# Optimization experiments

Hardware: AMD Instinct MI355X
Metric: run time of the kernel (lower is better)

## Reference

```python
import jax, jax.numpy as jnp
import numpy as np

SCALE, R_MAX, ALPHA = 16, 8, 2.0
HL, WL, C_FEAT = 16, 16, 384
HH, WH = HL * SCALE, WL * SCALE


def bilinear_resize(img, out_h, out_w):
    """PyTorch F.interpolate(mode='bilinear', align_corners=False, antialias=False).
    img: [..., H, W] -> [..., out_h, out_w]."""
    H, W = img.shape[-2], img.shape[-1]
    ys = jnp.maximum((jnp.arange(out_h, dtype=jnp.float32) + 0.5) * (H / out_h) - 0.5, 0.0)
    xs = jnp.maximum((jnp.arange(out_w, dtype=jnp.float32) + 0.5) * (W / out_w) - 0.5, 0.0)
    y0 = jnp.floor(ys).astype(jnp.int32)
    x0 = jnp.floor(xs).astype(jnp.int32)
    y1 = jnp.minimum(y0 + 1, H - 1)
    x1 = jnp.minimum(x0 + 1, W - 1)
    wy = (ys - y0)[:, None]
    wx = (xs - x0)[None, :]
    g = lambda yi, xi: img[..., yi[:, None], xi[None, :]]
    return ((1 - wy) * (1 - wx) * g(y0, x0) + (1 - wy) * wx * g(y0, x1)
            + wy * (1 - wx) * g(y1, x0) + wy * wx * g(y1, x1))


def jbu_forward(feat_lr, guide_hr, sx_raw, sy_raw, th_raw, sr_raw):
    C, Hl, Wl = feat_lr.shape[1], feat_lr.shape[2], feat_lr.shape[3]
    Hh, Wh = guide_hr.shape[2], guide_hr.shape[3]
    scale, R_max, alpha = SCALE, R_MAX, ALPHA
    NEG = -1e30  # finite stand-in for -inf (keeps grads NaN-free)

    # parameter transforms from the module
    sx = jnp.exp(sx_raw[0, 0])
    sy = jnp.exp(sy_raw[0, 0])
    th = jnp.pi * jnp.tanh(th_raw[0, 0])
    sr = jnp.exp(sr_raw[0, 0])

    Y, X = jnp.meshgrid(jnp.arange(Hh, dtype=jnp.float32),
                        jnp.arange(Wh, dtype=jnp.float32), indexing='ij')
    u = (Y + 0.5) / scale - 0.5
    v = (X + 0.5) / scale - 0.5
    uc = jnp.clip(jnp.round(u), 0, Hl - 1).astype(jnp.int32)
    vc = jnp.clip(jnp.round(v), 0, Wl - 1).astype(jnp.int32)

    sigma_eff_hr = bilinear_resize(jnp.maximum(sx, sy), Hh, Wh)
    R_map = jnp.clip(jnp.ceil(alpha * sigma_eff_hr), 1.0, float(R_max))  # [Hh,Wh]

    offs = jnp.arange(-R_max, R_max + 1, dtype=jnp.int32)
    dYg, dXg = jnp.meshgrid(offs, offs, indexing='ij')
    dY = dYg.reshape(-1)[:, None, None]  # [N,1,1]
    dX = dXg.reshape(-1)[:, None, None]

    Ui = jnp.clip(uc[None] + dY, 0, Hl - 1)  # [N,Hh,Wh]
    Vi = jnp.clip(vc[None] + dX, 0, Wl - 1)
    idx = Ui * Wl + Vi                       # flat LR index per (neighbor, HR pixel)
    gat = lambda mp: mp.reshape(-1)[idx]

    sxg = jnp.maximum(gat(sx), 1e-6)
    syg = jnp.maximum(gat(sy), 1e-6)
    thg = gat(th)
    srg = jnp.maximum(gat(sr), 1e-6)

    dx = X[None] - ((Vi.astype(jnp.float32) + 0.5) * scale - 0.5)
    dyv = Y[None] - ((Ui.astype(jnp.float32) + 0.5) * scale - 0.5)
    ct, st = jnp.cos(thg), jnp.sin(thg)
    a = dx * ct + dyv * st
    b = -dx * st + dyv * ct

    guide_lr = bilinear_resize(guide_hr[0], Hl, Wl)  # [3,Hl,Wl]
    g_diff2 = sum((guide_hr[0, c][None] - gat(guide_lr[c])) ** 2 for c in range(3))

    log_w = (-a * a / (2 * sxg ** 2 + 1e-8)
             - b * b / (2 * syg ** 2 + 1e-8)
             - g_diff2 / (2.0 * srg ** 2 + 1e-8))  # [N,Hh,Wh]

    mask = (dY * dY + dX * dX).astype(jnp.float32) <= R_map[None] ** 2
    log_w = jnp.where(mask, log_w, NEG)

    # numerically stable softmax over neighbors (== online-softmax result)
    m = log_w.max(axis=0)
    s = jnp.exp(log_w - m[None])  # masked entries underflow to 0
    den = s.sum(axis=0)           # [Hh,Wh]

    # num[c,h,w] = sum_n s[n,h,w] * feat[idx[n,h,w], c]
    # scatter neighbor weights by LR pixel, then one GEMM with the LR features
    N = idx.shape[0]
    idx2 = idx.reshape(N, Hh * Wh)
    cols = jnp.arange(Hh * Wh, dtype=jnp.int32)[None, :]
    acc = jnp.zeros((Hl * Wl, Hh * Wh), jnp.float32).at[idx2, cols].add(s.reshape(N, -1))
    feat_flat = feat_lr[0].reshape(C, Hl * Wl)  # [C, P]
    num = jnp.einsum('cp,pq->cq', feat_flat, acc).reshape(C, Hh, Wh)

    return (num / jnp.maximum(den, 1e-8)[None])[None]  # [1,C,Hh,Wh]


def setup_inputs() -> dict:
    key = jax.random.key(0)
    k1, k2, k3, k4, k5, k6 = jax.random.split(key, 6)
    feat_lr = jax.random.normal(k1, (1, C_FEAT, HL, WL), jnp.float32)
    guide_hr = jax.random.uniform(k2, (1, 3, HH, WH), dtype=jnp.float32)
    log_sigma = float(np.log(16.0))
    log_sigma_r = float(np.log(0.12))
    sx_raw = log_sigma + 0.1 * jax.random.normal(k3, (1, 1, HL, WL), jnp.float32)
    sy_raw = log_sigma + 0.1 * jax.random.normal(k4, (1, 1, HL, WL), jnp.float32)
    th_raw = 0.1 * jax.random.normal(k5, (1, 1, HL, WL), jnp.float32)
    sr_raw = log_sigma_r + 0.1 * jax.random.normal(k6, (1, 1, HL, WL), jnp.float32)
    return {"feat_lr": feat_lr, "guide_hr": guide_hr, "sx_raw": sx_raw,
            "sy_raw": sy_raw, "th_raw": th_raw, "sr_raw": sr_raw}


def reference(feat_lr, guide_hr, sx_raw, sy_raw, th_raw, sr_raw):
    return jbu_forward(feat_lr, guide_hr, sx_raw, sy_raw, th_raw, sr_raw)
```

## Files before the change

kernel.cpp:

```cpp
#include <hip/hip_runtime.h>
#include <math.h>

#define NEG_BIG  (-1e30f)
#define NEG_H16  (-60000.0f)

typedef _Float16 half8  __attribute__((ext_vector_type(8)));
typedef _Float16 half2v __attribute__((ext_vector_type(2)));
typedef float    floatx4 __attribute__((ext_vector_type(4)));

__global__ __launch_bounds__(256) void setup_all(
    const float* __restrict__ feat, const float* __restrict__ guide,
    const float* __restrict__ sx_raw, const float* __restrict__ sy_raw,
    const float* __restrict__ th_raw, const float* __restrict__ sr_raw,
    _Float16* __restrict__ feat16, float4* __restrict__ PA,
    float4* __restrict__ PB, float* __restrict__ PS,
    _Float16* __restrict__ LCtab)
{
    const int b = blockIdx.x, t = threadIdx.x;
    if (b < 48) {
        int i = (b*256 + t)*8;
        float4 f0 = *(const float4*)(feat + i);
        float4 f1 = *(const float4*)(feat + i + 4);
        half8 h;
        h[0]=(_Float16)f0.x; h[1]=(_Float16)f0.y; h[2]=(_Float16)f0.z; h[3]=(_Float16)f0.w;
        h[4]=(_Float16)f1.x; h[5]=(_Float16)f1.y; h[6]=(_Float16)f1.z; h[7]=(_Float16)f1.w;
        *(half8*)(feat16 + i) = h;
        return;
    }
    if (b == 48) {
        float sx = expf(sx_raw[t]);
        float sy = expf(sy_raw[t]);
        float th = 3.14159265358979323846f * tanhf(th_raw[t]);
        float sr = expf(sr_raw[t]);
        float sxg = fmaxf(sx, 1e-6f), syg = fmaxf(sy, 1e-6f), srg = fmaxf(sr, 1e-6f);
        float iA = 1.f / (2.f*sxg*sxg + 1e-8f);
        float iB = 1.f / (2.f*syg*syg + 1e-8f);
        float iC = 1.f / (2.f*srg*srg + 1e-8f);
        float ct = cosf(th), st = sinf(th);
        float A2 = iA*ct*ct + iB*st*st;
        float B2 = 2.f*ct*st*(iA - iB);
        float C2 = iA*st*st + iB*ct*ct;
        PA[t] = make_float4(-A2, -B2, -C2, -iC);
        int i = t >> 4, j = t & 15;
        int y0 = 16*i + 7, x0 = 16*j + 7;
        float g[3];
#pragma unroll
        for (int c = 0; c < 3; ++c) {
            const float* gp = guide + c*65536;
            g[c] = 0.25f*(gp[y0*256 + x0]     + gp[y0*256 + x0 + 1] +
                          gp[(y0+1)*256 + x0] + gp[(y0+1)*256 + x0 + 1]);
        }
        PB[t] = make_float4(2.f*iC*g[0], 2.f*iC*g[1], 2.f*iC*g[2],
                            -iC*(g[0]*g[0] + g[1]*g[1] + g[2]*g[2]));
        PS[t] = fmaxf(sx, sy);
        return;
    }
    const int tb  = b - 49;
    const int uc  = tb >> 2;
    const int vc0 = (tb & 3) << 2;
    const int Pu  = t >> 4;
    const int colb = t & 15;
    int ylo = (Pu == 0)  ? -8 : (Pu - uc);
    int yhi = (Pu == 15) ?  8 : (Pu - uc);
    ylo = max(ylo, -8); yhi = min(yhi, 8);
    _Float16* dst = LCtab + (size_t)tb * 8192;
#pragma unroll
    for (int h = 0; h < 2; ++h) {
        const int col32 = colb + h*16;
        const int Rt = (col32 >> 2) + 1;
        const int vc = vc0 + (col32 & 3);
        const int R2 = Rt * Rt;
        int cnt[16];
#pragma unroll
        for (int Pv = 1; Pv < 15; ++Pv) {
            int d = Pv - vc;
            int lim = R2 - d*d;
            int c = 0;
            if (lim >= 0 && ylo <= yhi) {
                int s = (int)sqrtf((float)lim);
                c = max(0, min(yhi, s) - max(ylo, -s) + 1);
            }
            cnt[Pv] = c;
        }
        cnt[0] = 0;
        if (-vc >= -8) {
            for (int dY = ylo; dY <= yhi; ++dY) {
                int lim = R2 - dY*dY;
                if (lim >= 0) {
                    int r = (int)sqrtf((float)lim);
                    cnt[0] += max(0, min(-vc, r) + r + 1);
                }
            }
        }
        cnt[15] = 0;
        if (15 - vc <= 8) {
            for (int dY = ylo; dY <= yhi; ++dY) {
                int lim = R2 - dY*dY;
                if (lim >= 0) {
                    int r = (int)sqrtf((float)lim);
                    cnt[15] += max(0, r - max(15 - vc, -r) + 1);
                }
            }
        }
#pragma unroll
        for (int Pv = 0; Pv < 16; ++Pv)
            dst[(Pu*16 + Pv)*32 + col32] = (_Float16)
                ((cnt[Pv] > 0) ? __logf((float)cnt[Pv]) : NEG_H16);
    }
}

__global__ __launch_bounds__(1024, 8) void jbu_main(
    const float* __restrict__ guide, const _Float16* __restrict__ feat16,
    const float4* __restrict__ PA, const float4* __restrict__ PB,
    const float* __restrict__ PS, const _Float16* __restrict__ LCtab,
    float* __restrict__ out)
{
    __shared__ __align__(16) _Float16 Wb[64][256];
    __shared__ float redM[16][64];
    __shared__ float redD[16][64];

    const int t  = threadIdx.x;
    const int q  = t & 63;
    const int wv = t >> 6;
    const int grpu = __builtin_amdgcn_readfirstlane(wv);

    const int n   = blockIdx.x;
    const int xcd = n & 7;
    const int s   = n >> 3;
    const int Y   = xcd*32 + (s >> 2);
    const int X0  = (s & 3) << 6;
    const int X   = X0 + q;
    const float Yf = (float)Y, Xf = (float)X;
    const int uc   = Y >> 4;

    float u = (Yf + 0.5f)*0.0625f - 0.5f;
    float v = (Xf + 0.5f)*0.0625f - 0.5f;
    float ysc = fmaxf(u, 0.f), xsc = fmaxf(v, 0.f);
    int y0 = (int)ysc, x0 = (int)xsc;
    int y1 = min(y0 + 1, 15), x1 = min(x0 + 1, 15);
    float wy = ysc - (float)y0, wx = xsc - (float)x0;
    float s00 = PS[y0*16 + x0], s01 = PS[y0*16 + x1];
    float s10 = PS[y1*16 + x0], s11 = PS[y1*16 + x1];
    float sig = (1.f - wy)*((1.f - wx)*s00 + wx*s01)
              +        wy *((1.f - wx)*s10 + wx*s11);
    float Rf = fminf(fmaxf(ceilf(2.f*sig), 1.f), 8.f);
    const int colq = ((int)Rf - 1)*4 + (q >> 4);

    const float g0 = guide[          (Y << 8) + X];
    const float g1 = guide[ 65536 + ((Y << 8) + X)];
    const float g2 = guide[131072 + ((Y << 8) + X)];
    const float g2s = g0*g0 + g1*g1 + g2*g2;

    const _Float16* Lb = LCtab + (size_t)(uc*4 + (X0 >> 6))*8192 + colq;

    const int pbase = grpu << 4;
    const float dy  = Yf - (16.f*(float)grpu + 7.5f);
    const float dy2 = dy*dy;
    float lw[16];
    float mloc = NEG_BIG;
#pragma unroll
    for (int col = 0; col < 16; ++col) {
        int p = pbase + col;
        float dx = Xf - (16.f*(float)col + 7.5f);
        float4 A = PA[p];
        float4 B = PB[p];
        float w = fmaf(B.x, g0, B.w);
        w = fmaf(B.y, g1, w);
        w = fmaf(B.z, g2, w);
        w = fmaf(A.w, g2s, w);
        w = fmaf(A.x, dx*dx, w);
        w = fmaf(A.y, dx*dy, w);
        w = fmaf(A.z, dy2, w);
        w += (float)Lb[p*32];
        lw[col] = w;
        mloc = fmaxf(mloc, w);
    }
    redM[wv][q] = mloc;
    __syncthreads();
    float m = redM[0][q];
#pragma unroll
    for (int k = 1; k < 16; ++k) m = fmaxf(m, redM[k][q]);

    float dloc = 0.f;
#pragma unroll
    for (int col = 0; col < 16; col += 2) {
        int p0 = pbase + col;
        float e0 = __expf(lw[col]     - m);
        float e1 = __expf(lw[col + 1] - m);
        half2v hh; hh[0] = (_Float16)e0; hh[1] = (_Float16)e1;
        int chunk = ((p0 >> 3) ^ q) & 31;
        *(half2v*)&Wb[q][chunk*8 + (p0 & 7)] = hh;
        dloc += (float)hh[0] + (float)hh[1];
    }
    redD[wv][q] = dloc;
    __syncthreads();

    const int lane = t & 63;
    const int mrow = lane & 15;
    const int quad = lane >> 4;
    const int cg   = grpu >> 1;
    const int ph   = grpu & 1;
    const int c0   = cg * 48;
    const int pixbase = ph * 32;

    float idv[2];
#pragma unroll
    for (int nt = 0; nt < 2; ++nt) {
        int pix = pixbase + nt*16 + mrow;
        float den = 0.f;
#pragma unroll
        for (int k = 0; k < 16; ++k) den += redD[k][pix];
        idv[nt] = 1.f / fmaxf(den, 1e-8f);
    }

    floatx4 acc[3][2] = {};
    const _Float16* fbase = feat16 + (c0 + mrow)*256 + quad*8;

#pragma unroll
    for (int ks = 0; ks < 8; ++ks) {
        half8 a[3];
#pragma unroll
        for (int mt = 0; mt < 3; ++mt)
            a[mt] = *(const half8*)(fbase + mt*16*256 + ks*32);
        half8 b[2];
#pragma unroll
        for (int nt = 0; nt < 2; ++nt) {
            int pix = pixbase + nt*16 + mrow;
            int chunk = ((ks*4 + quad) ^ pix) & 31;
            b[nt] = *(const half8*)(&Wb[pix][chunk*8]);
        }
#pragma unroll
        for (int mt = 0; mt < 3; ++mt)
#pragma unroll
            for (int nt = 0; nt < 2; ++nt)
                acc[mt][nt] = __builtin_amdgcn_mfma_f32_16x16x32_f16(
                    a[mt], b[nt], acc[mt][nt], 0, 0, 0);
    }

    __syncthreads();

    float* Sf = (float*)Wb + (grpu << 9);
    const int sch = lane >> 3;
    const int spg = lane & 7;
    const int outcol = (Y << 8) + X0 + pixbase;
#pragma unroll
    for (int mt = 0; mt < 3; ++mt) {
#pragma unroll
        for (int nt = 0; nt < 2; ++nt)
#pragma unroll
            for (int r = 0; r < 4; ++r)
                Sf[(quad*4 + r)*32 + nt*16 + mrow] = acc[mt][nt][r] * idv[nt];
#pragma unroll
        for (int j = 0; j < 2; ++j) {
            float4 vv = *(const float4*)&Sf[(j*8 + sch)*32 + spg*4];
            *(float4*)(out + (size_t)(c0 + mt*16 + j*8 + sch)*65536
                           + outcol + spg*4) = vv;
        }
    }
}

extern "C" void kernel_launch(void* const* d_in, const int* in_sizes, int n_in,
                              void* d_out, int out_size, void* d_ws, size_t ws_size,
                              hipStream_t stream)
{
    const float* feat   = (const float*)d_in[0];
    const float* guide  = (const float*)d_in[1];
    const float* sx_raw = (const float*)d_in[2];
    const float* sy_raw = (const float*)d_in[3];
    const float* th_raw = (const float*)d_in[4];
    const float* sr_raw = (const float*)d_in[5];
    float* out = (float*)d_out;

    char* ws = (char*)d_ws;
    _Float16* feat16 = (_Float16*)ws;
    float4*   PA     = (float4*)(ws + 196608);
    float4*   PB     = (float4*)(ws + 200704);
    float*    PS     = (float*)(ws + 204800);
    _Float16* LCtab  = (_Float16*)(ws + 205824);

    setup_all<<<113, 256, 0, stream>>>(feat, guide, sx_raw, sy_raw, th_raw,
                                       sr_raw, feat16, PA, PB, PS, LCtab);
    jbu_main<<<1024, 1024, 0, stream>>>(guide, feat16, PA, PB, PS, LCtab, out);
}
```

Before: 164.4 us.

## Split fused JBU kernel into weight-generation and GEMM kernels via global buffer

Splits the single fused kernel into two. The first computes the per-pixel softmax weights and inverse denominators and writes them to a 32 MB fp16 global buffer. The second performs the feature-by-weight MFMA GEMM per HR row with wider output tiles and row-contiguous stores. This aims to let each phase have its own occupancy and tiling and to write output more coalesced, at the cost of a large extra global write and read of the weights plus an additional launch.

Result: slower. 185.3 us (+12.7%).

```diff
diff --git a/kernel.cpp b/kernel.cpp
--- a/kernel.cpp
+++ b/kernel.cpp
@@ -109,11 +109,11 @@
     }
 }
 
-__global__ __launch_bounds__(1024, 8) void jbu_main(
-    const float* __restrict__ guide, const _Float16* __restrict__ feat16,
-    const float4* __restrict__ PA, const float4* __restrict__ PB,
-    const float* __restrict__ PS, const _Float16* __restrict__ LCtab,
-    float* __restrict__ out)
+__global__ __launch_bounds__(1024) void jbu_wden(
+    const float* __restrict__ guide, const float4* __restrict__ PA,
+    const float4* __restrict__ PB, const float* __restrict__ PS,
+    const _Float16* __restrict__ LCtab,
+    _Float16* __restrict__ Wg, float* __restrict__ invden)
 {
     __shared__ __align__(16) _Float16 Wb[64][256];
     __shared__ float redM[16][64];
@@ -125,10 +125,8 @@
     const int grpu = __builtin_amdgcn_readfirstlane(wv);
 
     const int n   = blockIdx.x;
-    const int xcd = n & 7;
-    const int s   = n >> 3;
-    const int Y   = xcd*32 + (s >> 2);
-    const int X0  = (s & 3) << 6;
+    const int Y   = n >> 2;
+    const int X0  = (n & 3) << 6;
     const int X   = X0 + q;
     const float Yf = (float)Y, Xf = (float)X;
     const int uc   = Y >> 4;
@@ -195,66 +193,99 @@
     redD[wv][q] = dloc;
     __syncthreads();
 
+    if (t < 64) {
+        float den = 0.f;
+#pragma unroll
+        for (int k = 0; k < 16; ++k) den += redD[k][t];
+        invden[(Y << 8) + X0 + t] = 1.f / fmaxf(den, 1e-8f);
+    }
+
+    {
+        const float4* src = (const float4*)((const char*)Wb + t*32);
+        float4* dst = (float4*)((char*)Wg
+                        + ((size_t)(Y << 8) + (size_t)X0)*512 + (size_t)t*32);
+        dst[0] = src[0];
+        dst[1] = src[1];
+    }
+}
+
+__global__ __launch_bounds__(1024) void jbu_gemm(
+    const _Float16* __restrict__ feat16, const _Float16* __restrict__ Wg,
+    const float* __restrict__ invden, float* __restrict__ out)
+{
+    __shared__ float Sf[32*264];
+
+    const int t    = threadIdx.x;
     const int lane = t & 63;
+    const int wv   = t >> 6;
     const int mrow = lane & 15;
     const int quad = lane >> 4;
-    const int cg   = grpu >> 1;
-    const int ph   = grpu & 1;
-    const int c0   = cg * 48;
-    const int pixbase = ph * 32;
-
-    float idv[2];
-#pragma unroll
-    for (int nt = 0; nt < 2; ++nt) {
-        int pix = pixbase + nt*16 + mrow;
-        float den = 0.f;
-#pragma unroll
-        for (int k = 0; k < 16; ++k) den += redD[k][pix];
-        idv[nt] = 1.f / fmaxf(den, 1e-8f);
-    }
-
-    floatx4 acc[3][2] = {};
-    const _Float16* fbase = feat16 + (c0 + mrow)*256 + quad*8;
-
-#pragma unroll
-    for (int ks = 0; ks < 8; ++ks) {
-        half8 a[3];
-#pragma unroll
-        for (int mt = 0; mt < 3; ++mt)
-            a[mt] = *(const half8*)(fbase + mt*16*256 + ks*32);
-        half8 b[2];
-#pragma unroll
-        for (int nt = 0; nt < 2; ++nt) {
-            int pix = pixbase + nt*16 + mrow;
-            int chunk = ((ks*4 + quad) ^ pix) & 31;
-            b[nt] = *(const half8*)(&Wb[pix][chunk*8]);
-        }
-#pragma unroll
-        for (int mt = 0; mt < 3; ++mt)
-#pragma unroll
-            for (int nt = 0; nt < 2; ++nt)
-                acc[mt][nt] = __builtin_amdgcn_mfma_f32_16x16x32_f16(
-                    a[mt], b[nt], acc[mt][nt], 0, 0, 0);
-    }
-
-    __syncthreads();
-
-    float* Sf = (float*)Wb + (grpu << 9);
-    const int sch = lane >> 3;
-    const int spg = lane & 7;
-    const int outcol = (Y << 8) + X0 + pixbase;
-#pragma unroll
-    for (int mt = 0; mt < 3; ++mt) {
-#pragma unroll
-        for (int nt = 0; nt < 2; ++nt)
-#pragma unroll
-            for (int r = 0; r < 4; ++r)
-                Sf[(quad*4 + r)*32 + nt*16 + mrow] = acc[mt][nt][r] * idv[nt];
-#pragma unroll
-        for (int j = 0; j < 2; ++j) {
-            float4 vv = *(const float4*)&Sf[(j*8 + sch)*32 + spg*4];
-            *(float4*)(out + (size_t)(c0 + mt*16 + j*8 + sch)*65536
-                           + outcol + spg*4) = vv;
+    const int cgw  = wv >> 2;
+    const int pq   = wv & 3;
+    const int Y    = blockIdx.x;
+    const int rowbase = Y << 8;
+
+    const _Float16* wrow[4];
+    float idv[4];
+    int cm[4];
+#pragma unroll
+    for (int nt = 0; nt < 4; ++nt) {
+        int pxl = pq*64 + nt*16 + mrow;
+        wrow[nt] = Wg + (((size_t)rowbase + pxl) << 8);
+        idv[nt]  = invden[rowbase + pxl];
+        cm[nt]   = pxl & 31;
+    }
+    const int chl_w = t >> 5;
+    const int xs    = t & 31;
+
+#pragma unroll
+    for (int pass = 0; pass < 2; ++pass) {
+        const int c0 = pass*192 + cgw*48;
+        floatx4 acc[3][4] = {};
+        const _Float16* fbase = feat16 + (c0 + mrow)*256 + quad*8;
+
+#pragma unroll
+        for (int ks = 0; ks < 8; ++ks) {
+            half8 a[3];
+#pragma unroll
+            for (int mt = 0; mt < 3; ++mt)
+                a[mt] = *(const half8*)(fbase + mt*4096 + ks*32);
+            half8 b[4];
+#pragma unroll
+            for (int nt = 0; nt < 4; ++nt)
+                b[nt] = *(const half8*)(wrow[nt] + (((ks*4 + quad) ^ cm[nt]) & 31)*8);
+#pragma unroll
+            for (int mt = 0; mt < 3; ++mt)
+#pragma unroll
+                for (int nt = 0; nt < 4; ++nt)
+                    acc[mt][nt] = __builtin_amdgcn_mfma_f32_16x16x32_f16(
+                        a[mt], b[nt], acc[mt][nt], 0, 0, 0);
+        }
+
+#pragma unroll
+        for (int h = 0; h < 2; ++h) {
+#pragma unroll
+            for (int mt = 0; mt < 3; ++mt) {
+                __syncthreads();
+                if ((cgw >> 1) == h) {
+                    const int chl = (cgw & 1)*16 + quad*4;
+#pragma unroll
+                    for (int nt = 0; nt < 4; ++nt)
+#pragma unroll
+                        for (int r = 0; r < 4; ++r)
+                            Sf[(chl + r)*264 + pq*64 + nt*16 + mrow] =
+                                acc[mt][nt][r] * idv[nt];
+                }
+                __syncthreads();
+                const float* sp = &Sf[chl_w*264 + xs*8];
+                float4 v0 = *(const float4*)sp;
+                float4 v1 = *(const float4*)(sp + 4);
+                const int c = pass*192 + (2*h + (chl_w >> 4))*48
+                            + mt*16 + (chl_w & 15);
+                float* dp = out + ((size_t)c << 16) + rowbase + xs*8;
+                *(float4*)dp       = v0;
+                *(float4*)(dp + 4) = v1;
+            }
         }
     }
 }
@@ -277,8 +308,11 @@
     float4*   PB     = (float4*)(ws + 200704);
     float*    PS     = (float*)(ws + 204800);
     _Float16* LCtab  = (_Float16*)(ws + 205824);
+    _Float16* Wg     = (_Float16*)(ws + 1254400);
+    float*    invden = (float*)(ws + 1254400 + 33554432);
 
     setup_all<<<113, 256, 0, stream>>>(feat, guide, sx_raw, sy_raw, th_raw,
                                        sr_raw, feat16, PA, PB, PS, LCtab);
-    jbu_main<<<1024, 1024, 0, stream>>>(guide, feat16, PA, PB, PS, LCtab, out);
+    jbu_wden<<<1024, 1024, 0, stream>>>(guide, PA, PB, PS, LCtab, Wg, invden);
+    jbu_gemm<<<256, 1024, 0, stream>>>(feat16, Wg, invden, out);
 }
```

## Stage output through shared memory in channel rounds and simplify block mapping

Applied to the files above, without the earlier changes.

The epilogue now writes the accumulators into a padded shared tile in four rounds. Each round covers 96 channels, and all 16 waves then store one full 64-pixel row segment per channel with scalar coalesced stores. Previously each wave staged and stored its own 16x32 sub-tile as float4s. The block-to-row mapping drops the XCD-aware swizzle in favour of a plain linear mapping, and the launch bounds no longer request 8 waves per EU. The change adds extra block-wide barriers per round and gives up the XCD locality of the old mapping.

After: 163.9 us. No clear change (-0.3%).

```diff
diff --git a/kernel.cpp b/kernel.cpp
--- a/kernel.cpp
+++ b/kernel.cpp
@@ -109,7 +109,7 @@
     }
 }
 
-__global__ __launch_bounds__(1024, 8) void jbu_main(
+__global__ __launch_bounds__(1024) void jbu_main(
     const float* __restrict__ guide, const _Float16* __restrict__ feat16,
     const float4* __restrict__ PA, const float4* __restrict__ PB,
     const float* __restrict__ PS, const _Float16* __restrict__ LCtab,
@@ -125,10 +125,8 @@
     const int grpu = __builtin_amdgcn_readfirstlane(wv);
 
     const int n   = blockIdx.x;
-    const int xcd = n & 7;
-    const int s   = n >> 3;
-    const int Y   = xcd*32 + (s >> 2);
-    const int X0  = (s & 3) << 6;
+    const int Y   = n >> 2;
+    const int X0  = (n & 3) << 6;
     const int X   = X0 + q;
     const float Yf = (float)Y, Xf = (float)X;
     const int uc   = Y >> 4;
@@ -237,24 +235,29 @@
                     a[mt], b[nt], acc[mt][nt], 0, 0, 0);
     }
 
-    __syncthreads();
-
-    float* Sf = (float*)Wb + (grpu << 9);
-    const int sch = lane >> 3;
-    const int spg = lane & 7;
-    const int outcol = (Y << 8) + X0 + pixbase;
-#pragma unroll
-    for (int mt = 0; mt < 3; ++mt) {
-#pragma unroll
-        for (int nt = 0; nt < 2; ++nt)
-#pragma unroll
-            for (int r = 0; r < 4; ++r)
-                Sf[(quad*4 + r)*32 + nt*16 + mrow] = acc[mt][nt][r] * idv[nt];
-#pragma unroll
-        for (int j = 0; j < 2; ++j) {
-            float4 vv = *(const float4*)&Sf[(j*8 + sch)*32 + spg*4];
-            *(float4*)(out + (size_t)(c0 + mt*16 + j*8 + sch)*65536
-                           + outcol + spg*4) = vv;
+    float* Sf = (float*)Wb;
+    const size_t outrow = (size_t)(Y << 8) + X0;
+#pragma unroll
+    for (int r = 0; r < 4; ++r) {
+        __syncthreads();
+        if ((cg >> 1) == r) {
+            const int cb = (cg & 1)*48;
+#pragma unroll
+            for (int mt = 0; mt < 3; ++mt)
+#pragma unroll
+                for (int nt = 0; nt < 2; ++nt) {
+                    const int px = pixbase + nt*16 + mrow;
+#pragma unroll
+                    for (int rr = 0; rr < 4; ++rr)
+                        Sf[(cb + mt*16 + quad*4 + rr)*68 + px] =
+                            acc[mt][nt][rr] * idv[nt];
+                }
+        }
+        __syncthreads();
+#pragma unroll
+        for (int k = 0; k < 6; ++k) {
+            const int cl = grpu*6 + k;
+            out[(size_t)(r*96 + cl)*65536 + outrow + lane] = Sf[cl*68 + lane];
         }
     }
 }
```
